# Optimization experiments

Hardware: AMD Instinct MI355X
Metric: run time of the kernel (lower is better)

Reference implementation:

```python
import math
import jax, jax.numpy as jnp
import numpy as np

DIM = 1024
HEADS = 16
KV_HEADS = 4            # use_mqa: heads // 4
HEAD_DIM = DIM // HEADS  # 64
KV_DIM = KV_HEADS * HEAD_DIM  # 256
WINDOW = 64
SCALE = HEAD_DIM ** -0.5


def _alibi_slopes(n_heads: int) -> np.ndarray:
    # n_heads is a power of 2 here
    start = 2.0 ** (-(2.0 ** (-(math.log2(n_heads) - 3))))
    return np.array([start * (start ** i) for i in range(n_heads)], dtype=np.float32)


def setup_inputs() -> dict:
    key = jax.random.key(0)
    ks = jax.random.split(key, 5)
    B, N = 1, 2048
    x = jax.random.normal(ks[0], (B, N, DIM), dtype=jnp.float32)
    # Linear weights stored as [in, out] (applied as x @ W)
    sq = 1.0 / math.sqrt(DIM)
    Wq = jax.random.uniform(ks[1], (DIM, DIM), jnp.float32, -sq, sq)
    Wk = jax.random.uniform(ks[2], (DIM, KV_DIM), jnp.float32, -sq, sq)
    Wv = jax.random.uniform(ks[3], (DIM, KV_DIM), jnp.float32, -sq, sq)
    Wo = jax.random.uniform(ks[4], (DIM, DIM), jnp.float32, -sq, sq)
    return {"x": x, "Wq": Wq, "Wk": Wk, "Wv": Wv, "Wo": Wo}


def reference(x, Wq, Wk, Wv, Wo):
    B, N, C = x.shape
    # projections -> [B, H, N, hd]
    q = (x @ Wq).reshape(B, N, HEADS, HEAD_DIM).transpose(0, 2, 1, 3)
    k = (x @ Wk).reshape(B, N, KV_HEADS, HEAD_DIM).transpose(0, 2, 1, 3)
    v = (x @ Wv).reshape(B, N, KV_HEADS, HEAD_DIM).transpose(0, 2, 1, 3)
    # MQA: repeat kv heads (torch repeat_interleave on head dim)
    rep = HEADS // KV_HEADS
    k = jnp.repeat(k, rep, axis=1)
    v = jnp.repeat(v, rep, axis=1)

    scores = jnp.einsum("bhqd,bhkd->bhqk", q, k) * SCALE  # [B,H,N,N]

    # ALiBi bias: distance[i, j] = j - i, scaled per head
    idx = jnp.arange(N)
    dist = (idx[None, :] - idx[:, None]).astype(scores.dtype)  # [N, N]
    slopes = jnp.asarray(_alibi_slopes(HEADS))                 # [H]
    scores = scores + dist[None, None, :, :] * slopes[None, :, None, None]

    # causal AND local band (|i-j| <= WINDOW) -> allowed iff j in [i-WINDOW, i]
    causal = idx[None, :] <= idx[:, None]
    band = jnp.abs(idx[:, None] - idx[None, :]) <= WINDOW
    allowed = causal & band  # [N, N]
    scores_local = jnp.where(allowed[None, None], scores, -jnp.inf)
    attn_local = jax.nn.softmax(scores_local, axis=-1)
    out_local = jnp.einsum("bhqk,bhkd->bhqd", attn_local, v)

    # global: strided keys every WINDOW positions, full (non-causal) softmax
    k_g = k[:, :, ::WINDOW, :]
    v_g = v[:, :, ::WINDOW, :]
    scores_g = jnp.einsum("bhqd,bhkd->bhqk", q, k_g) * SCALE
    attn_g = jax.nn.softmax(scores_g, axis=-1)
    out_global = jnp.einsum("bhqk,bhkd->bhqd", attn_g, v_g)

    out = (out_local + out_global).transpose(0, 2, 1, 3).reshape(B, N, C)
    return out @ Wo
```

## Files before the change

### kernel.cpp

```cpp
#include <hip/hip_runtime.h>

#define SCALE 0.125f

typedef unsigned short ushort_t;
typedef unsigned short ushortx8 __attribute__((ext_vector_type(8)));
typedef unsigned short ushortx4 __attribute__((ext_vector_type(4)));
typedef short bf16x8 __attribute__((ext_vector_type(8)));
typedef float f32x4 __attribute__((ext_vector_type(4)));

__device__ inline ushort_t f2bf(float f) {
  unsigned int u = __float_as_uint(f);
  u += 0x7FFFu + ((u >> 16) & 1u);
  return (ushort_t)(u >> 16);
}
__device__ inline float bf2f(ushort_t u) {
  return __uint_as_float(((unsigned int)u) << 16);
}

__global__ __launch_bounds__(256) void prep_kernel(
    const float* __restrict__ x, const float* __restrict__ Wq, const float* __restrict__ Wk,
    const float* __restrict__ Wv, const float* __restrict__ Wo,
    ushort_t* __restrict__ x_bf, ushort_t* __restrict__ wqkv_t, ushort_t* __restrict__ wo_t)
{
  __shared__ float t[64][65];
  int bid = blockIdx.x;
  const int tid = threadIdx.x;
  if (bid < 2048) {
    int idx = (bid * 256 + tid) * 4;
    if (idx < 2048 * 1024) {
      float4 f = *(const float4*)(x + idx);
      ushortx4 o = { f2bf(f.x), f2bf(f.y), f2bf(f.z), f2bf(f.w) };
      *(ushortx4*)(x_bf + idx) = o;
    }
    return;
  }
  bid -= 2048;
  const float* src; int C; ushort_t* dst; int row_off, cb, kb;
  if (bid < 256)      { src = Wq; C = 1024; dst = wqkv_t; row_off = 0;    cb = bid & 15; kb = bid >> 4; }
  else if (bid < 320) { int j = bid - 256; src = Wk; C = 256; dst = wqkv_t; row_off = 1024; cb = j & 3; kb = j >> 2; }
  else if (bid < 384) { int j = bid - 320; src = Wv; C = 256; dst = wqkv_t; row_off = 1280; cb = j & 3; kb = j >> 2; }
  else                { int j = bid - 384; src = Wo; C = 1024; dst = wo_t; row_off = 0;    cb = j & 15; kb = j >> 4; }
  const int c0 = cb * 64, k0 = kb * 64;
  const int c = tid & 63, r4 = tid >> 6;
  for (int rr = r4; rr < 64; rr += 4)
    t[c][rr] = src[(size_t)(k0 + rr) * C + c0 + c];
  __syncthreads();
  const int kk = tid & 63, n4 = tid >> 6;
  for (int nn = n4; nn < 64; nn += 4)
    dst[(size_t)(row_off + c0 + nn) * 1024 + k0 + kk] = f2bf(t[nn][kk]);
}

__global__ __launch_bounds__(256) void gemm_qkv_kernel(
    const ushort_t* __restrict__ A, const ushort_t* __restrict__ Bt,
    ushort_t* __restrict__ qout, ushort_t* __restrict__ kout, ushort_t* __restrict__ vout)
{
  __shared__ __align__(16) ushort_t lA[128 * 32];
  __shared__ __align__(16) ushort_t lB[128 * 32];
  const int tid = threadIdx.x;
  const int lane = tid & 63;
  const int quad = lane >> 4;
  const int l16 = lane & 15;
  const int wid = tid >> 6;
  const int rw = (wid >> 1) * 64, cw = (wid & 1) * 64;
  const int m0 = blockIdx.y * 128, n0 = blockIdx.x * 128;

  const int e0 = tid * 8;
  const int r0 = e0 >> 5, c0 = e0 & 31;
  const int e1 = e0 + 2048;
  const int r1 = e1 >> 5, c1 = e1 & 31;

  const ushort_t* Ab = A + (size_t)m0 * 1024;
  const ushort_t* Bb = Bt + (size_t)n0 * 1024;

  f32x4 acc[4][4] = {};

  for (int k0 = 0; k0 < 1024; k0 += 32) {
    __syncthreads();
    __builtin_amdgcn_global_load_lds(
        (const __attribute__((address_space(1))) unsigned int*)(Ab + (size_t)r0 * 1024 + k0 + c0),
        (__attribute__((address_space(3))) unsigned int*)(lA + e0), 16, 0, 0);
    __builtin_amdgcn_global_load_lds(
        (const __attribute__((address_space(1))) unsigned int*)(Ab + (size_t)r1 * 1024 + k0 + c1),
        (__attribute__((address_space(3))) unsigned int*)(lA + e1), 16, 0, 0);
    __builtin_amdgcn_global_load_lds(
        (const __attribute__((address_space(1))) unsigned int*)(Bb + (size_t)r0 * 1024 + k0 + c0),
        (__attribute__((address_space(3))) unsigned int*)(lB + e0), 16, 0, 0);
    __builtin_amdgcn_global_load_lds(
        (const __attribute__((address_space(1))) unsigned int*)(Bb + (size_t)r1 * 1024 + k0 + c1),
        (__attribute__((address_space(3))) unsigned int*)(lB + e1), 16, 0, 0);
    __syncthreads();

    bf16x8 bfr[4];
#pragma unroll
    for (int ni = 0; ni < 4; ++ni)
      bfr[ni] = *(const bf16x8*)(lB + (cw + ni * 16 + l16) * 32 + quad * 8);
#pragma unroll
    for (int mi = 0; mi < 4; ++mi) {
      bf16x8 afr = *(const bf16x8*)(lA + (rw + mi * 16 + l16) * 32 + quad * 8);
#pragma unroll
      for (int ni = 0; ni < 4; ++ni)
        acc[mi][ni] = __builtin_amdgcn_mfma_f32_16x16x32_bf16(afr, bfr[ni], acc[mi][ni], 0, 0, 0);
    }
  }

#pragma unroll
  for (int mi = 0; mi < 4; ++mi) {
#pragma unroll
    for (int ni = 0; ni < 4; ++ni) {
#pragma unroll
      for (int r = 0; r < 4; ++r) {
        int row = m0 + rw + mi * 16 + quad * 4 + r;
        int col = n0 + cw + ni * 16 + l16;
        float v = acc[mi][ni][r];
        if (col < 1024)      qout[(size_t)row * 1024 + col] = f2bf(v);
        else if (col < 1280) kout[(size_t)row * 256 + (col - 1024)] = f2bf(v);
        else                 vout[(size_t)row * 256 + (col - 1280)] = f2bf(v);
      }
    }
  }
}

__global__ __launch_bounds__(256) void attn_mfma_kernel(
    const ushort_t* __restrict__ Q, const ushort_t* __restrict__ Kb,
    const ushort_t* __restrict__ Vb, ushort_t* __restrict__ O)
{
  __shared__ __align__(16) ushort_t lK[128 * 64];
  __shared__ __align__(16) ushort_t lVt[64 * 128];
  __shared__ __align__(16) ushort_t lKg[32 * 64];
  __shared__ __align__(16) ushort_t lVtg[64 * 40];
  __shared__ __align__(16) ushort_t lP[64 * 128];
  __shared__ __align__(16) ushort_t lPg[64 * 40];

  const int h = blockIdx.x, qb = blockIdx.y;
  const int tid = threadIdx.x;
  const int kvcol = (h >> 2) * 64;
  const int kbase = qb * 64 - 64;

  for (int cidx = tid; cidx < 1024; cidx += 256) {
    const int key = cidx >> 3, ch = cidx & 7;
    const int kpos = kbase + key;
    ushortx8 kv = {0,0,0,0,0,0,0,0}, vv = {0,0,0,0,0,0,0,0};
    if (kpos >= 0) {
      kv = *(const ushortx8*)(Kb + (size_t)kpos * 256 + kvcol + ch * 8);
      vv = *(const ushortx8*)(Vb + (size_t)kpos * 256 + kvcol + ch * 8);
    }
    *(ushortx8*)(lK + key * 64 + ((ch ^ (key & 7)) << 3)) = kv;
    const int kc = key >> 3, ke = key & 7;
#pragma unroll
    for (int e = 0; e < 8; ++e) {
      int dim = ch * 8 + e;
      lVt[dim * 128 + ((kc ^ (dim & 7)) << 3) + ke] = vv[e];
    }
  }
  {
    const int g = tid >> 3, ch = tid & 7;
    const int kpos = g * 64;
    ushortx8 kv = *(const ushortx8*)(Kb + (size_t)kpos * 256 + kvcol + ch * 8);
    ushortx8 vv = *(const ushortx8*)(Vb + (size_t)kpos * 256 + kvcol + ch * 8);
    *(ushortx8*)(lKg + g * 64 + ((ch ^ (g & 7)) << 3)) = kv;
#pragma unroll
    for (int e = 0; e < 8; ++e) lVtg[(ch * 8 + e) * 40 + g] = vv[e];
  }
  __syncthreads();

  const int lane = tid & 63, w = tid >> 6;
  const int quad = lane >> 4, l16 = lane & 15;
  const int l7 = l16 & 7;
  const float slope = exp2f(-0.5f * (float)(h + 1));

  const int qrow = qb * 64 + w * 16 + l16;
  const ushort_t* qptr = Q + (size_t)qrow * 1024 + h * 64 + quad * 8;
  const bf16x8 aq0 = *(const bf16x8*)(qptr);
  const bf16x8 aq1 = *(const bf16x8*)(qptr + 32);

  float s[8][4];
#pragma unroll
  for (int kt = 0; kt < 8; ++kt) {
    const int key = kt * 16 + l16;
    const bf16x8 b0 = *(const bf16x8*)(lK + key * 64 + ((quad ^ l7) << 3));
    const bf16x8 b1 = *(const bf16x8*)(lK + key * 64 + (((4 + quad) ^ l7) << 3));
    f32x4 acc = {0.f, 0.f, 0.f, 0.f};
    acc = __builtin_amdgcn_mfma_f32_16x16x32_bf16(aq0, b0, acc, 0, 0, 0);
    acc = __builtin_amdgcn_mfma_f32_16x16x32_bf16(aq1, b1, acc, 0, 0, 0);
    const int kpos = kbase + key;
#pragma unroll
    for (int r = 0; r < 4; ++r) {
      const int qp = qb * 64 + w * 16 + quad * 4 + r;
      const int d = kpos - qp;
      const bool ok = (d <= 0) && (d >= -64) && (kpos >= 0);
      s[kt][r] = ok ? acc[r] * SCALE + (float)d * slope : -1e30f;
    }
  }
  float mr[4] = {-1e30f, -1e30f, -1e30f, -1e30f};
#pragma unroll
  for (int kt = 0; kt < 8; ++kt)
#pragma unroll
    for (int r = 0; r < 4; ++r) mr[r] = fmaxf(mr[r], s[kt][r]);
#pragma unroll
  for (int r = 0; r < 4; ++r) {
    mr[r] = fmaxf(mr[r], __shfl_xor(mr[r], 1));
    mr[r] = fmaxf(mr[r], __shfl_xor(mr[r], 2));
    mr[r] = fmaxf(mr[r], __shfl_xor(mr[r], 4));
    mr[r] = fmaxf(mr[r], __shfl_xor(mr[r], 8));
  }
  float lr[4] = {0.f, 0.f, 0.f, 0.f};
#pragma unroll
  for (int kt = 0; kt < 8; ++kt)
#pragma unroll
    for (int r = 0; r < 4; ++r) { float p = __expf(s[kt][r] - mr[r]); s[kt][r] = p; lr[r] += p; }
#pragma unroll
  for (int r = 0; r < 4; ++r) {
    lr[r] += __shfl_xor(lr[r], 1);
    lr[r] += __shfl_xor(lr[r], 2);
    lr[r] += __shfl_xor(lr[r], 4);
    lr[r] += __shfl_xor(lr[r], 8);
    lr[r] = 1.f / lr[r];
  }
#pragma unroll
  for (int kt = 0; kt < 8; ++kt) {
    const int kc = kt * 2 + (l16 >> 3);
#pragma unroll
    for (int r = 0; r < 4; ++r) {
      const int qr = w * 16 + quad * 4 + r;
      lP[qr * 128 + ((kc ^ (qr & 7)) << 3) + l7] = f2bf(s[kt][r] * lr[r]);
    }
  }

  float sg[2][4];
#pragma unroll
  for (int g16 = 0; g16 < 2; ++g16) {
    const int key = g16 * 16 + l16;
    const bf16x8 b0 = *(const bf16x8*)(lKg + key * 64 + ((quad ^ l7) << 3));
    const bf16x8 b1 = *(const bf16x8*)(lKg + key * 64 + (((4 + quad) ^ l7) << 3));
    f32x4 acc = {0.f, 0.f, 0.f, 0.f};
    acc = __builtin_amdgcn_mfma_f32_16x16x32_bf16(aq0, b0, acc, 0, 0, 0);
    acc = __builtin_amdgcn_mfma_f32_16x16x32_bf16(aq1, b1, acc, 0, 0, 0);
#pragma unroll
    for (int r = 0; r < 4; ++r) sg[g16][r] = acc[r] * SCALE;
  }
  float mg[4], lg[4];
#pragma unroll
  for (int r = 0; r < 4; ++r) {
    mg[r] = fmaxf(sg[0][r], sg[1][r]);
    mg[r] = fmaxf(mg[r], __shfl_xor(mg[r], 1));
    mg[r] = fmaxf(mg[r], __shfl_xor(mg[r], 2));
    mg[r] = fmaxf(mg[r], __shfl_xor(mg[r], 4));
    mg[r] = fmaxf(mg[r], __shfl_xor(mg[r], 8));
  }
#pragma unroll
  for (int r = 0; r < 4; ++r) {
    float p0 = __expf(sg[0][r] - mg[r]);
    float p1 = __expf(sg[1][r] - mg[r]);
    sg[0][r] = p0; sg[1][r] = p1;
    lg[r] = p0 + p1;
    lg[r] += __shfl_xor(lg[r], 1);
    lg[r] += __shfl_xor(lg[r], 2);
    lg[r] += __shfl_xor(lg[r], 4);
    lg[r] += __shfl_xor(lg[r], 8);
    lg[r] = 1.f / lg[r];
  }
#pragma unroll
  for (int g16 = 0; g16 < 2; ++g16)
#pragma unroll
    for (int r = 0; r < 4; ++r) {
      const int qr = w * 16 + quad * 4 + r;
      lPg[qr * 40 + g16 * 16 + l16] = f2bf(sg[g16][r] * lg[r]);
    }

  f32x4 acco[4] = {};
  const int qA = w * 16 + l16;
#pragma unroll
  for (int kki = 0; kki < 4; ++kki) {
    const bf16x8 ap = *(const bf16x8*)(lP + qA * 128 + (((kki * 4 + quad) ^ l7) << 3));
#pragma unroll
    for (int nt = 0; nt < 4; ++nt) {
      const int dim = nt * 16 + l16;
      const bf16x8 bv = *(const bf16x8*)(lVt + dim * 128 + (((kki * 4 + quad) ^ l7) << 3));
      acco[nt] = __builtin_amdgcn_mfma_f32_16x16x32_bf16(ap, bv, acco[nt], 0, 0, 0);
    }
  }
  {
    const bf16x8 apg = *(const bf16x8*)(lPg + qA * 40 + quad * 8);
#pragma unroll
    for (int nt = 0; nt < 4; ++nt) {
      const bf16x8 bvg = *(const bf16x8*)(lVtg + (nt * 16 + l16) * 40 + quad * 8);
      acco[nt] = __builtin_amdgcn_mfma_f32_16x16x32_bf16(apg, bvg, acco[nt], 0, 0, 0);
    }
  }
#pragma unroll
  for (int nt = 0; nt < 4; ++nt)
#pragma unroll
    for (int r = 0; r < 4; ++r) {
      const int qp = qb * 64 + w * 16 + quad * 4 + r;
      O[(size_t)qp * 1024 + h * 64 + nt * 16 + l16] = f2bf(acco[nt][r]);
    }
}

__global__ __launch_bounds__(256) void gemm_out_kernel(
    const ushort_t* __restrict__ A, const ushort_t* __restrict__ Bt, float* __restrict__ fout)
{
  __shared__ __align__(16) ushort_t lA[128 * 32];
  __shared__ __align__(16) ushort_t lB[64 * 32];
  const int tid = threadIdx.x;
  const int lane = tid & 63, wid = tid >> 6;
  const int quad = lane >> 4, l16 = lane & 15;
  const int m0 = blockIdx.y * 128, n0 = blockIdx.x * 64;
  const int e0 = tid * 8, r0 = e0 >> 5, c0 = e0 & 31;
  const int e1 = e0 + 2048, r1 = e1 >> 5, c1 = e1 & 31;
  const ushort_t* Ab = A + (size_t)m0 * 1024;
  const ushort_t* Bb = Bt + (size_t)n0 * 1024;

  f32x4 acc[2][4] = {};

  for (int k0 = 0; k0 < 1024; k0 += 32) {
    __syncthreads();
    __builtin_amdgcn_global_load_lds(
        (const __attribute__((address_space(1))) unsigned int*)(Ab + (size_t)r0 * 1024 + k0 + c0),
        (__attribute__((address_space(3))) unsigned int*)(lA + e0), 16, 0, 0);
    __builtin_amdgcn_global_load_lds(
        (const __attribute__((address_space(1))) unsigned int*)(Ab + (size_t)r1 * 1024 + k0 + c1),
        (__attribute__((address_space(3))) unsigned int*)(lA + e1), 16, 0, 0);
    __builtin_amdgcn_global_load_lds(
        (const __attribute__((address_space(1))) unsigned int*)(Bb + (size_t)r0 * 1024 + k0 + c0),
        (__attribute__((address_space(3))) unsigned int*)(lB + e0), 16, 0, 0);
    __syncthreads();

    bf16x8 bfr[4];
#pragma unroll
    for (int ni = 0; ni < 4; ++ni)
      bfr[ni] = *(const bf16x8*)(lB + (ni * 16 + l16) * 32 + quad * 8);
#pragma unroll
    for (int mi = 0; mi < 2; ++mi) {
      bf16x8 afr = *(const bf16x8*)(lA + (wid * 32 + mi * 16 + l16) * 32 + quad * 8);
#pragma unroll
      for (int ni = 0; ni < 4; ++ni)
        acc[mi][ni] = __builtin_amdgcn_mfma_f32_16x16x32_bf16(afr, bfr[ni], acc[mi][ni], 0, 0, 0);
    }
  }

#pragma unroll
  for (int mi = 0; mi < 2; ++mi)
#pragma unroll
    for (int ni = 0; ni < 4; ++ni)
#pragma unroll
      for (int r = 0; r < 4; ++r) {
        int row = m0 + wid * 32 + mi * 16 + quad * 4 + r;
        int col = n0 + ni * 16 + l16;
        fout[(size_t)row * 1024 + col] = acc[mi][ni][r];
      }
}

extern "C" void kernel_launch(void* const* d_in, const int* in_sizes, int n_in,
                              void* d_out, int out_size, void* d_ws, size_t ws_size,
                              hipStream_t stream)
{
  const float* x  = (const float*)d_in[0];
  const float* Wq = (const float*)d_in[1];
  const float* Wk = (const float*)d_in[2];
  const float* Wv = (const float*)d_in[3];
  const float* Wo = (const float*)d_in[4];
  float* out = (float*)d_out;

  char* ws = (char*)d_ws;
  ushort_t* x_bf   = (ushort_t*)(ws);
  ushort_t* wqkv_t = (ushort_t*)(ws + (4ull  << 20));
  ushort_t* wo_t   = (ushort_t*)(ws + (7ull  << 20));
  ushort_t* q_bf   = (ushort_t*)(ws + (9ull  << 20));
  ushort_t* k_bf   = (ushort_t*)(ws + (13ull << 20));
  ushort_t* v_bf   = (ushort_t*)(ws + (14ull << 20));
  ushort_t* at_bf  = (ushort_t*)(ws + (15ull << 20));

  prep_kernel<<<2688, 256, 0, stream>>>(x, Wq, Wk, Wv, Wo, x_bf, wqkv_t, wo_t);
  gemm_qkv_kernel<<<dim3(12, 16), 256, 0, stream>>>(x_bf, wqkv_t, q_bf, k_bf, v_bf);
  attn_mfma_kernel<<<dim3(16, 32), 256, 0, stream>>>(q_bf, k_bf, v_bf, at_bf);
  gemm_out_kernel<<<dim3(16, 16), 256, 0, stream>>>(at_bf, wo_t, out);
}
```

Measured before the change: 125.6 us.

## Unify projection GEMMs into 64x64-tile kernel with swizzled LDS and XCD mapping

New measurement: 109.9 us. 1.14x faster.

```diff
diff --git a/kernel.cpp b/kernel.cpp
--- a/kernel.cpp
+++ b/kernel.cpp
@@ -50,74 +50,78 @@
     dst[(size_t)(row_off + c0 + nn) * 1024 + k0 + kk] = f2bf(t[nn][kk]);
 }
 
-__global__ __launch_bounds__(256) void gemm_qkv_kernel(
-    const ushort_t* __restrict__ A, const ushort_t* __restrict__ Bt,
-    ushort_t* __restrict__ qout, ushort_t* __restrict__ kout, ushort_t* __restrict__ vout)
+__global__ __launch_bounds__(256) void gemm64_kernel(
+    const ushort_t* __restrict__ A, const ushort_t* __restrict__ Bt, int mode, int ntn,
+    ushort_t* __restrict__ qout, ushort_t* __restrict__ kout, ushort_t* __restrict__ vout,
+    float* __restrict__ fout)
 {
-  __shared__ __align__(16) ushort_t lA[128 * 32];
-  __shared__ __align__(16) ushort_t lB[128 * 32];
+  __shared__ __align__(16) ushort_t lA[64 * 64];
+  __shared__ __align__(16) ushort_t lB[64 * 64];
+  const int bid = blockIdx.x;
+  const int xcd = bid & 7, g = bid >> 3;
+  const int m0 = (xcd + 8 * (g / ntn)) * 64;
+  const int n0 = (g % ntn) * 64;
+
   const int tid = threadIdx.x;
-  const int lane = tid & 63;
-  const int quad = lane >> 4;
-  const int l16 = lane & 15;
-  const int wid = tid >> 6;
-  const int rw = (wid >> 1) * 64, cw = (wid & 1) * 64;
-  const int m0 = blockIdx.y * 128, n0 = blockIdx.x * 128;
-
-  const int e0 = tid * 8;
-  const int r0 = e0 >> 5, c0 = e0 & 31;
-  const int e1 = e0 + 2048;
-  const int r1 = e1 >> 5, c1 = e1 & 31;
-
-  const ushort_t* Ab = A + (size_t)m0 * 1024;
-  const ushort_t* Bb = Bt + (size_t)n0 * 1024;
-
-  f32x4 acc[4][4] = {};
-
-  for (int k0 = 0; k0 < 1024; k0 += 32) {
+  const int lane = tid & 63, w = tid >> 6;
+  const int quad = lane >> 4, l16 = lane & 15;
+  const int rw = (w >> 1) * 32, cw = (w & 1) * 32;
+
+  const int rs = tid >> 3;
+  const int swz = (tid & 7) ^ (rs & 7);
+  const int eL = tid * 8;
+  const ushort_t* Ab = A + (size_t)(m0 + rs) * 1024 + swz * 8;
+  const ushort_t* Bb = Bt + (size_t)(n0 + rs) * 1024 + swz * 8;
+
+  const int xa = l16 & 7;
+  f32x4 acc[2][2] = {};
+
+  for (int k0 = 0; k0 < 1024; k0 += 64) {
     __syncthreads();
     __builtin_amdgcn_global_load_lds(
-        (const __attribute__((address_space(1))) unsigned int*)(Ab + (size_t)r0 * 1024 + k0 + c0),
-        (__attribute__((address_space(3))) unsigned int*)(lA + e0), 16, 0, 0);
+        (const __attribute__((address_space(1))) unsigned int*)(Ab + k0),
+        (__attribute__((address_space(3))) unsigned int*)(lA + eL), 16, 0, 0);
     __builtin_amdgcn_global_load_lds(
-        (const __attribute__((address_space(1))) unsigned int*)(Ab + (size_t)r1 * 1024 + k0 + c1),
-        (__attribute__((address_space(3))) unsigned int*)(lA + e1), 16, 0, 0);
+        (const __attribute__((address_space(1))) unsigned int*)(Ab + 32 * 1024 + k0),
+        (__attribute__((address_space(3))) unsigned int*)(lA + eL + 2048), 16, 0, 0);
     __builtin_amdgcn_global_load_lds(
-        (const __attribute__((address_space(1))) unsigned int*)(Bb + (size_t)r0 * 1024 + k0 + c0),
-        (__attribute__((address_space(3))) unsigned int*)(lB + e0), 16, 0, 0);
+        (const __attribute__((address_space(1))) unsigned int*)(Bb + k0),
+        (__attribute__((address_space(3))) unsigned int*)(lB + eL), 16, 0, 0);
     __builtin_amdgcn_global_load_lds(
-        (const __attribute__((address_space(1))) unsigned int*)(Bb + (size_t)r1 * 1024 + k0 + c1),
-        (__attribute__((address_space(3))) unsigned int*)(lB + e1), 16, 0, 0);
+        (const __attribute__((address_space(1))) unsigned int*)(Bb + 32 * 1024 + k0),
+        (__attribute__((address_space(3))) unsigned int*)(lB + eL + 2048), 16, 0, 0);
     __syncthreads();
 
-    bf16x8 bfr[4];
-#pragma unroll
-    for (int ni = 0; ni < 4; ++ni)
-      bfr[ni] = *(const bf16x8*)(lB + (cw + ni * 16 + l16) * 32 + quad * 8);
-#pragma unroll
-    for (int mi = 0; mi < 4; ++mi) {
-      bf16x8 afr = *(const bf16x8*)(lA + (rw + mi * 16 + l16) * 32 + quad * 8);
-#pragma unroll
-      for (int ni = 0; ni < 4; ++ni)
-        acc[mi][ni] = __builtin_amdgcn_mfma_f32_16x16x32_bf16(afr, bfr[ni], acc[mi][ni], 0, 0, 0);
-    }
-  }
-
-#pragma unroll
-  for (int mi = 0; mi < 4; ++mi) {
-#pragma unroll
-    for (int ni = 0; ni < 4; ++ni) {
+#pragma unroll
+    for (int kh = 0; kh < 2; ++kh) {
+      bf16x8 a0 = *(const bf16x8*)(lA + (rw + l16) * 64      + (((kh * 4 + quad) ^ xa) << 3));
+      bf16x8 a1 = *(const bf16x8*)(lA + (rw + 16 + l16) * 64 + (((kh * 4 + quad) ^ xa) << 3));
+      bf16x8 b0 = *(const bf16x8*)(lB + (cw + l16) * 64      + (((kh * 4 + quad) ^ xa) << 3));
+      bf16x8 b1 = *(const bf16x8*)(lB + (cw + 16 + l16) * 64 + (((kh * 4 + quad) ^ xa) << 3));
+      acc[0][0] = __builtin_amdgcn_mfma_f32_16x16x32_bf16(a0, b0, acc[0][0], 0, 0, 0);
+      acc[0][1] = __builtin_amdgcn_mfma_f32_16x16x32_bf16(a0, b1, acc[0][1], 0, 0, 0);
+      acc[1][0] = __builtin_amdgcn_mfma_f32_16x16x32_bf16(a1, b0, acc[1][0], 0, 0, 0);
+      acc[1][1] = __builtin_amdgcn_mfma_f32_16x16x32_bf16(a1, b1, acc[1][1], 0, 0, 0);
+    }
+  }
+
+#pragma unroll
+  for (int mg = 0; mg < 2; ++mg)
+#pragma unroll
+    for (int ng = 0; ng < 2; ++ng)
 #pragma unroll
       for (int r = 0; r < 4; ++r) {
-        int row = m0 + rw + mi * 16 + quad * 4 + r;
-        int col = n0 + cw + ni * 16 + l16;
-        float v = acc[mi][ni][r];
-        if (col < 1024)      qout[(size_t)row * 1024 + col] = f2bf(v);
-        else if (col < 1280) kout[(size_t)row * 256 + (col - 1024)] = f2bf(v);
-        else                 vout[(size_t)row * 256 + (col - 1280)] = f2bf(v);
+        const int row = m0 + rw + mg * 16 + quad * 4 + r;
+        const int col = n0 + cw + ng * 16 + l16;
+        const float v = acc[mg][ng][r];
+        if (mode == 0) {
+          if (n0 < 1024)       qout[(size_t)row * 1024 + col] = f2bf(v);
+          else if (n0 < 1280)  kout[(size_t)row * 256 + (col - 1024)] = f2bf(v);
+          else                 vout[(size_t)row * 256 + (col - 1280)] = f2bf(v);
+        } else {
+          fout[(size_t)row * 1024 + col] = v;
+        }
       }
-    }
-  }
 }
 
 __global__ __launch_bounds__(256) void attn_mfma_kernel(
@@ -153,13 +157,13 @@
     }
   }
   {
-    const int g = tid >> 3, ch = tid & 7;
-    const int kpos = g * 64;
+    const int gk = tid >> 3, ch = tid & 7;
+    const int kpos = gk * 64;
     ushortx8 kv = *(const ushortx8*)(Kb + (size_t)kpos * 256 + kvcol + ch * 8);
     ushortx8 vv = *(const ushortx8*)(Vb + (size_t)kpos * 256 + kvcol + ch * 8);
-    *(ushortx8*)(lKg + g * 64 + ((ch ^ (g & 7)) << 3)) = kv;
-#pragma unroll
-    for (int e = 0; e < 8; ++e) lVtg[(ch * 8 + e) * 40 + g] = vv[e];
+    *(ushortx8*)(lKg + gk * 64 + ((ch ^ (gk & 7)) << 3)) = kv;
+#pragma unroll
+    for (int e = 0; e < 8; ++e) lVtg[(ch * 8 + e) * 40 + gk] = vv[e];
   }
   __syncthreads();
 
@@ -296,60 +300,6 @@
     }
 }
 
-__global__ __launch_bounds__(256) void gemm_out_kernel(
-    const ushort_t* __restrict__ A, const ushort_t* __restrict__ Bt, float* __restrict__ fout)
-{
-  __shared__ __align__(16) ushort_t lA[128 * 32];
-  __shared__ __align__(16) ushort_t lB[64 * 32];
-  const int tid = threadIdx.x;
-  const int lane = tid & 63, wid = tid >> 6;
-  const int quad = lane >> 4, l16 = lane & 15;
-  const int m0 = blockIdx.y * 128, n0 = blockIdx.x * 64;
-  const int e0 = tid * 8, r0 = e0 >> 5, c0 = e0 & 31;
-  const int e1 = e0 + 2048, r1 = e1 >> 5, c1 = e1 & 31;
-  const ushort_t* Ab = A + (size_t)m0 * 1024;
-  const ushort_t* Bb = Bt + (size_t)n0 * 1024;
-
-  f32x4 acc[2][4] = {};
-
-  for (int k0 = 0; k0 < 1024; k0 += 32) {
-    __syncthreads();
-    __builtin_amdgcn_global_load_lds(
-        (const __attribute__((address_space(1))) unsigned int*)(Ab + (size_t)r0 * 1024 + k0 + c0),
-        (__attribute__((address_space(3))) unsigned int*)(lA + e0), 16, 0, 0);
-    __builtin_amdgcn_global_load_lds(
-        (const __attribute__((address_space(1))) unsigned int*)(Ab + (size_t)r1 * 1024 + k0 + c1),
-        (__attribute__((address_space(3))) unsigned int*)(lA + e1), 16, 0, 0);
-    __builtin_amdgcn_global_load_lds(
-        (const __attribute__((address_space(1))) unsigned int*)(Bb + (size_t)r0 * 1024 + k0 + c0),
-        (__attribute__((address_space(3))) unsigned int*)(lB + e0), 16, 0, 0);
-    __syncthreads();
-
-    bf16x8 bfr[4];
-#pragma unroll
-    for (int ni = 0; ni < 4; ++ni)
-      bfr[ni] = *(const bf16x8*)(lB + (ni * 16 + l16) * 32 + quad * 8);
-#pragma unroll
-    for (int mi = 0; mi < 2; ++mi) {
-      bf16x8 afr = *(const bf16x8*)(lA + (wid * 32 + mi * 16 + l16) * 32 + quad * 8);
-#pragma unroll
-      for (int ni = 0; ni < 4; ++ni)
-        acc[mi][ni] = __builtin_amdgcn_mfma_f32_16x16x32_bf16(afr, bfr[ni], acc[mi][ni], 0, 0, 0);
-    }
-  }
-
-#pragma unroll
-  for (int mi = 0; mi < 2; ++mi)
-#pragma unroll
-    for (int ni = 0; ni < 4; ++ni)
-#pragma unroll
-      for (int r = 0; r < 4; ++r) {
-        int row = m0 + wid * 32 + mi * 16 + quad * 4 + r;
-        int col = n0 + ni * 16 + l16;
-        fout[(size_t)row * 1024 + col] = acc[mi][ni][r];
-      }
-}
-
 extern "C" void kernel_launch(void* const* d_in, const int* in_sizes, int n_in,
                               void* d_out, int out_size, void* d_ws, size_t ws_size,
                               hipStream_t stream)
@@ -371,7 +321,7 @@
   ushort_t* at_bf  = (ushort_t*)(ws + (15ull << 20));
 
   prep_kernel<<<2688, 256, 0, stream>>>(x, Wq, Wk, Wv, Wo, x_bf, wqkv_t, wo_t);
-  gemm_qkv_kernel<<<dim3(12, 16), 256, 0, stream>>>(x_bf, wqkv_t, q_bf, k_bf, v_bf);
+  gemm64_kernel<<<768, 256, 0, stream>>>(x_bf, wqkv_t, 0, 24, q_bf, k_bf, v_bf, nullptr);
   attn_mfma_kernel<<<dim3(16, 32), 256, 0, stream>>>(q_bf, k_bf, v_bf, at_bf);
-  gemm_out_kernel<<<dim3(16, 16), 256, 0, stream>>>(at_bf, wo_t, out);
-}
+  gemm64_kernel<<<512, 256, 0, stream>>>(at_bf, wo_t, 1, 16, nullptr, nullptr, nullptr, out);
+}
```
